# Optimization experiments

Hardware: AMD Instinct MI355X
Metric: run time of the kernel (lower is better)

The kernel has to match this reference:

```python
import jax, jax.numpy as jnp
import numpy as np

# norse LIFParameters defaults
ALPHA = 100.0        # superspike surrogate slope
DT = 1e-3
TAU_SYN_INV = 200.0  # 1/5e-3
TAU_MEM_INV = 100.0  # 1/1e-2
V_TH = 1.0           # v_leak = v_reset = 0

@jax.custom_vjp
def heaviside(v):
    # forward: hard threshold; backward: superspike surrogate 1/(alpha*|v|+1)^2
    return (v > 0).astype(v.dtype)

def _hv_fwd(v):
    return heaviside(v), v

def _hv_bwd(v, g):
    return (g / (ALPHA * jnp.abs(v) + 1.0) ** 2,)

heaviside.defvjp(_hv_fwd, _hv_bwd)

def setup_inputs() -> dict:
    key = jax.random.key(0)
    ks = jax.random.split(key, 5)
    B, H, W, O = 2048, 15, 15, 10
    x = jax.random.uniform(ks[0], (B, 1, H, W), jnp.float32)  # image-like in [0,1)
    conv_w = jax.random.normal(ks[1], (2, 1, 4, 4), jnp.float32) * 0.25
    conv_b = jax.random.normal(ks[2], (2,), jnp.float32) * 0.1
    lin_w = jax.random.normal(ks[3], (O, 72), jnp.float32) * (1.0 / np.sqrt(72.0))
    lin_b = jax.random.normal(ks[4], (O,), jnp.float32) * 0.1
    return {"x": x, "conv_w": conv_w, "conv_b": conv_b,
            "lin_w": lin_w, "lin_b": lin_b, "num_steps": 300}

def reference(x, conv_w, conv_b, lin_w, lin_b, num_steps):
    B = x.shape[0]
    O = lin_w.shape[0]
    current = x * 10.0  # constant input current to the encoder

    def step(carry, _):
        v_enc, v, i = carry
        # --- constant_current_lif_encode step (lif_current_encoder) ---
        v_enc = v_enc + DT * TAU_MEM_INV * (-v_enc + current)
        z_in = heaviside(v_enc - V_TH)
        v_enc = v_enc - z_in * v_enc  # reset to v_reset = 0
        # --- feed-forward: conv -> maxpool(2) -> linear ---
        c = jax.lax.conv_general_dilated(
            z_in, conv_w, (1, 1), 'VALID',
            dimension_numbers=('NCHW', 'OIHW', 'NCHW')) + conv_b[None, :, None, None]
        p = jax.lax.reduce_window(c, -jnp.inf, jax.lax.max,
                                  (1, 1, 2, 2), (1, 1, 2, 2), 'VALID')  # [B,2,6,6]
        lin = p.reshape(B, -1) @ lin_w.T + lin_b  # [B,O]
        # --- norse LIFCell (lif_feed_forward_step) ---
        v_dec = v + DT * TAU_MEM_INV * (-v + i)
        i_dec = i - DT * TAU_SYN_INV * i
        spk = heaviside(v_dec - V_TH)
        v_new = (1.0 - spk) * v_dec  # v_reset = 0
        i_new = i_dec + lin
        return (v_enc, v_new, i_new), (spk, v_new)

    init = (jnp.zeros_like(current),
            jnp.zeros((B, O), x.dtype),
            jnp.zeros((B, O), x.dtype))
    _, (spk_rec, mem_rec) = jax.lax.scan(step, init, None, length=num_steps)
    spk_out = spk_rec.sum(0)  # [B,O]
    return spk_out, mem_rec, spk_rec
```

## Files before the change

### kernel.cpp

```cpp
#include <hip/hip_runtime.h>
#include <math.h>


typedef float v2f __attribute__((ext_vector_type(2)));

__global__ __launch_bounds__(128, 4) void snn_step_kernel(
    const float* __restrict__ x,
    const float* __restrict__ conv_w,
    const float* __restrict__ conv_b,
    const float* __restrict__ lin_w,
    const float* __restrict__ lin_b,
    float* __restrict__ out,
    int T, int B)
{
    const int b   = blockIdx.x;
    const int tid = threadIdx.x;
    const int w   = tid & 63;
    const int wv  = tid >> 6;

    __shared__ float    s_linw[720];
    __shared__ float    s_linb[10];
    __shared__ float4   s_lut[4][32];
    __shared__ uint4    s_bits4[16][8];
    __shared__ float    s_p[16][80];

    for (int j = tid; j < 720; j += 128) s_linw[j] = lin_w[j];
    if (tid < 10) s_linb[tid] = lin_b[tid];
    {
        const int ky = tid >> 5, n = tid & 31;
        float s00 = 0.f, s01 = 0.f, s10 = 0.f, s11 = 0.f;
#pragma unroll
        for (int kx = 0; kx < 4; ++kx) {
            const float w0 = conv_w[ky * 4 + kx];
            const float w1 = conv_w[16 + ky * 4 + kx];
            if ((n >> kx) & 1)       { s00 += w0; s01 += w1; }
            if ((n >> (kx + 1)) & 1) { s10 += w0; s11 += w1; }
        }
        s_lut[ky][n] = make_float4(s00, s01, s10, s11);
    }
    __syncthreads();

    v2f ve01 = (v2f){0.f, 0.f}, ve23 = (v2f){0.f, 0.f};
    v2f cur01, cur23;
    {
        const int jrow = w >> 4, col = w & 15;
        float c[4];
#pragma unroll
        for (int k = 0; k < 4; ++k) {
            const int  row = 4 * k + jrow;
            const bool act = (col < 15) && (row < 15) && (wv == 0);
            c[k] = act ? __fmul_rn(x[(size_t)b * 225 + row * 15 + col], 10.0f) : 0.f;
        }
        cur01 = (v2f){c[0], c[1]};
        cur23 = (v2f){c[2], c[3]};
    }

    const int  jword   = (w >> 2) + (w & 3);
    const bool wr_bits = (w < 24);

    const bool convlane = (w < 36);
    const int  py = w / 6, px = w - 6 * py;
    const int  wordsel = py;
    const int  shx = 2 * px, shx16 = shx + 16;
    const int  poff = 20 * (w / 9) + 2 * (w - 9 * (w / 9));
    const v2f  cb2 = (v2f){conv_b[0], conv_b[1]};

    const int lo = w >> 2, lq = w & 3;
    v2f lw2[9];
#pragma unroll
    for (int t = 0; t < 9; ++t) {
        int i0 = lo * 72 + 9 * lq + t;
        int i1 = i0 + 36;
        lw2[t] = (v2f){s_linw[i0 < 720 ? i0 : 719],
                       s_linw[i1 < 720 ? i1 : 719]};
    }
    const float lbias = s_linb[lo < 10 ? lo : 0];
    float v = 0.f, i_syn = 0.f, sc = 0.f;
    float svv[6], svs[6];
    const size_t BO = (size_t)B * 10;
    float* mp  = out + BO + (size_t)b * 10 + lo;
    float* spp = out + BO + (size_t)T * BO + (size_t)b * 10 + lo;

    auto enc_pack = [&](int slot) {
        const v2f tenth = (v2f){0.1f, 0.1f};
        v2f vn01 = ve01 + (cur01 - ve01) * tenth;
        v2f vn23 = ve23 + (cur23 - ve23) * tenth;
        bool sp0 = (vn01.x > 1.0f);
        bool sp1 = (vn01.y > 1.0f);
        bool sp2 = (vn23.x > 1.0f);
        bool sp3 = (vn23.y > 1.0f);
        unsigned long long bal0 = __ballot(sp0);
        unsigned long long bal1 = __ballot(sp1);
        unsigned long long bal2 = __ballot(sp2);
        unsigned long long bal3 = __ballot(sp3);
        ve01 = (v2f){sp0 ? 0.f : vn01.x, sp1 ? 0.f : vn01.y};
        ve23 = (v2f){sp2 ? 0.f : vn23.x, sp3 ? 0.f : vn23.y};
        const int jh = jword >> 1;
        unsigned long long m01 = (jh & 1) ? bal1 : bal0;
        unsigned long long m23 = (jh & 1) ? bal3 : bal2;
        unsigned long long m   = (jh & 2) ? m23 : m01;
        unsigned word = (unsigned)((jword & 1) ? (m >> 32) : m);
        word = (jword < 8) ? word : 0u;
        if (wr_bits) ((unsigned*)&s_bits4[slot][0])[w] = word;
    };

    auto conv_compute = [&](int slot, unsigned wb0, unsigned wb1, unsigned wb2) {
        const int i0 = (wb0 >> shx)   & 31;
        const int i1 = (wb0 >> shx16) & 31;
        const int i2 = (wb1 >> shx)   & 31;
        const int i3 = (wb1 >> shx16) & 31;
        const int i4 = (wb2 >> shx)   & 31;

        const float4 f0 = s_lut[0][i0];
        const float4 f1 = s_lut[1][i1];
        const float4 f2 = s_lut[2][i2];
        const float4 f3 = s_lut[3][i3];
        const float4 g0 = s_lut[0][i1];
        const float4 g1 = s_lut[1][i2];
        const float4 g2 = s_lut[2][i3];
        const float4 g3 = s_lut[3][i4];

        v2f a00 = (v2f){f0.x, f0.y};  a00 += (v2f){f1.x, f1.y};
        a00 += (v2f){f2.x, f2.y};     a00 += (v2f){f3.x, f3.y};
        v2f a01 = (v2f){f0.z, f0.w};  a01 += (v2f){f1.z, f1.w};
        a01 += (v2f){f2.z, f2.w};     a01 += (v2f){f3.z, f3.w};
        v2f a10 = (v2f){g0.x, g0.y};  a10 += (v2f){g1.x, g1.y};
        a10 += (v2f){g2.x, g2.y};     a10 += (v2f){g3.x, g3.y};
        v2f a11 = (v2f){g0.z, g0.w};  a11 += (v2f){g1.z, g1.w};
        a11 += (v2f){g2.z, g2.w};     a11 += (v2f){g3.z, g3.w};

        v2f mraw = __builtin_elementwise_max(
                       __builtin_elementwise_max(a00, a01),
                       __builtin_elementwise_max(a10, a11));
        v2f m2 = mraw + cb2;

        *(v2f*)&s_p[slot][poff] = m2;
    };

    auto lin_dec = [&](int s, int k) {
        const float* base = &s_p[s & 15][lq * 20];
        float4 q0 = *(const float4*)(base + 0);
        float4 q1 = *(const float4*)(base + 4);
        float4 q2 = *(const float4*)(base + 8);
        float4 q3 = *(const float4*)(base + 12);
        v2f    q4 = *(const v2f*)(base + 16);
        v2f pacc = (v2f){0.f, 0.f};
        pacc = __builtin_elementwise_fma(lw2[0], (v2f){q0.x, q0.y}, pacc);
        pacc = __builtin_elementwise_fma(lw2[1], (v2f){q0.z, q0.w}, pacc);
        pacc = __builtin_elementwise_fma(lw2[2], (v2f){q1.x, q1.y}, pacc);
        pacc = __builtin_elementwise_fma(lw2[3], (v2f){q1.z, q1.w}, pacc);
        pacc = __builtin_elementwise_fma(lw2[4], (v2f){q2.x, q2.y}, pacc);
        pacc = __builtin_elementwise_fma(lw2[5], (v2f){q2.z, q2.w}, pacc);
        pacc = __builtin_elementwise_fma(lw2[6], (v2f){q3.x, q3.y}, pacc);
        pacc = __builtin_elementwise_fma(lw2[7], (v2f){q3.z, q3.w}, pacc);
        pacc = __builtin_elementwise_fma(lw2[8], q4, pacc);
        float partial = __fadd_rn(pacc.x, pacc.y);

        float p1 = __shfl_xor(partial, 1);
        float p2 = __shfl_xor(partial, 2);
        float p3 = __shfl_xor(partial, 3);
        float lin = __fadd_rn(
            __fadd_rn(__fadd_rn(__fadd_rn(partial, p1), p2), p3), lbias);

        float vd  = __fadd_rn(v, __fmul_rn(0.1f, __fsub_rn(i_syn, v)));
        float id  = __fsub_rn(i_syn, __fmul_rn(0.2f, i_syn));
        float spk = (vd > 1.0f) ? 1.0f : 0.0f;
        v = (vd > 1.0f) ? 0.0f : vd;
        sc += spk;
        svv[k] = v;
        svs[k] = spk;
        i_syn = __fadd_rn(id, lin);
    };

    auto issue_stores = [&]() {
        if (lq == 0 && lo < 10) {
#pragma unroll
            for (int k = 0; k < 6; ++k) {
                mp[(size_t)k * BO]  = svv[k];
                spp[(size_t)k * BO] = svs[k];
            }
        }
        mp  += 6 * BO;
        spp += 6 * BO;
    };

    if (wv == 0) enc_pack(0);

    const int NG = T / 6;

    for (int g = 0; g < NG; ++g) {
        const int base = 6 * g;
        if (wv == 0) {
#pragma unroll
            for (int k = 0; k < 4; ++k) {
                const int s = base + k;
                uint4 bb = make_uint4(0, 0, 0, 0);
                if (convlane) bb = s_bits4[s & 15][wordsel];
                enc_pack((s + 1) & 15);
                if (convlane) conv_compute(s & 15, bb.x, bb.y, bb.z);
            }
            enc_pack((base + 5) & 15);
            enc_pack((base + 6) & 15);
        } else {
            if (g >= 2) issue_stores();
            if (g >= 1) {
                const int pb = base - 6;
                if (convlane) {
                    uint4 ba = s_bits4[(pb + 4) & 15][wordsel];
                    uint4 bc = s_bits4[(pb + 5) & 15][wordsel];
                    conv_compute((pb + 4) & 15, ba.x, ba.y, ba.z);
                    conv_compute((pb + 5) & 15, bc.x, bc.y, bc.z);
                }
#pragma unroll
                for (int k = 0; k < 6; ++k)
                    lin_dec(pb + k, k);
            }
        }
        __syncthreads();
    }

    if (wv == 1) {
        issue_stores();
        const int pb = 6 * (NG - 1);
        if (convlane) {
            uint4 ba = s_bits4[(pb + 4) & 15][wordsel];
            uint4 bc = s_bits4[(pb + 5) & 15][wordsel];
            conv_compute((pb + 4) & 15, ba.x, ba.y, ba.z);
            conv_compute((pb + 5) & 15, bc.x, bc.y, bc.z);
        }
#pragma unroll
        for (int k = 0; k < 6; ++k)
            lin_dec(pb + k, k);
        issue_stores();
        if (lq == 0 && lo < 10) out[(size_t)b * 10 + lo] = sc;
    }
}

extern "C" void kernel_launch(void* const* d_in, const int* in_sizes, int n_in,
                              void* d_out, int out_size, void* d_ws, size_t ws_size,
                              hipStream_t stream) {
    const float* x      = (const float*)d_in[0];
    const float* conv_w = (const float*)d_in[1];
    const float* conv_b = (const float*)d_in[2];
    const float* lin_w  = (const float*)d_in[3];
    const float* lin_b  = (const float*)d_in[4];
    float* out = (float*)d_out;

    const int B = in_sizes[0] / 225;
    const int T = (out_size / (B * 10) - 1) / 2;

    snn_step_kernel<<<B, 128, 0, stream>>>(x, conv_w, conv_b, lin_w, lin_b, out, T, B);
}
```

Before: 201.9 us.

## Restructure two-wave pipeline: encode a full group ahead, software-pipeline linear loads, DPP reductions

Wave 0 now encodes six future timesteps per group (after a six-step prologue and barrier) and batches its bit loads ahead of the conv work. Wave 1 computes the conv for steps 4-5 of the current group instead of the previous one, which shortens the dependency lag. Its linear-layer LDS loads are split from the math so the next step's loads are issued before the current step's FMAs. The quad-lane shuffles become DPP quad-permute moves, which avoids LDS-backed shuffles. The cost is more live registers and a different inter-wave schedule whose correctness relies on the 16-slot ring indexing.

```diff
diff --git a/kernel.cpp b/kernel.cpp
--- a/kernel.cpp
+++ b/kernel.cpp
@@ -3,6 +3,9 @@
 
 
 typedef float v2f __attribute__((ext_vector_type(2)));
+
+#define DPPQ(x, ctrl) \
+    __int_as_float(__builtin_amdgcn_mov_dpp(__float_as_int(x), (ctrl), 0xf, 0xf, true))
 
 __global__ __launch_bounds__(128, 4) void snn_step_kernel(
     const float* __restrict__ x,
@@ -137,28 +140,35 @@
         *(v2f*)&s_p[slot][poff] = m2;
     };
 
-    auto lin_dec = [&](int s, int k) {
-        const float* base = &s_p[s & 15][lq * 20];
-        float4 q0 = *(const float4*)(base + 0);
-        float4 q1 = *(const float4*)(base + 4);
-        float4 q2 = *(const float4*)(base + 8);
-        float4 q3 = *(const float4*)(base + 12);
-        v2f    q4 = *(const v2f*)(base + 16);
+    struct LinLd { float4 q0, q1, q2, q3; v2f q4; };
+
+    auto lin_load = [&](int s) {
+        LinLd L;
+        const float* pbase = &s_p[s & 15][lq * 20];
+        L.q0 = *(const float4*)(pbase + 0);
+        L.q1 = *(const float4*)(pbase + 4);
+        L.q2 = *(const float4*)(pbase + 8);
+        L.q3 = *(const float4*)(pbase + 12);
+        L.q4 = *(const v2f*)(pbase + 16);
+        return L;
+    };
+
+    auto lin_math = [&](const LinLd& L, int k) {
         v2f pacc = (v2f){0.f, 0.f};
-        pacc = __builtin_elementwise_fma(lw2[0], (v2f){q0.x, q0.y}, pacc);
-        pacc = __builtin_elementwise_fma(lw2[1], (v2f){q0.z, q0.w}, pacc);
-        pacc = __builtin_elementwise_fma(lw2[2], (v2f){q1.x, q1.y}, pacc);
-        pacc = __builtin_elementwise_fma(lw2[3], (v2f){q1.z, q1.w}, pacc);
-        pacc = __builtin_elementwise_fma(lw2[4], (v2f){q2.x, q2.y}, pacc);
-        pacc = __builtin_elementwise_fma(lw2[5], (v2f){q2.z, q2.w}, pacc);
-        pacc = __builtin_elementwise_fma(lw2[6], (v2f){q3.x, q3.y}, pacc);
-        pacc = __builtin_elementwise_fma(lw2[7], (v2f){q3.z, q3.w}, pacc);
-        pacc = __builtin_elementwise_fma(lw2[8], q4, pacc);
+        pacc = __builtin_elementwise_fma(lw2[0], (v2f){L.q0.x, L.q0.y}, pacc);
+        pacc = __builtin_elementwise_fma(lw2[1], (v2f){L.q0.z, L.q0.w}, pacc);
+        pacc = __builtin_elementwise_fma(lw2[2], (v2f){L.q1.x, L.q1.y}, pacc);
+        pacc = __builtin_elementwise_fma(lw2[3], (v2f){L.q1.z, L.q1.w}, pacc);
+        pacc = __builtin_elementwise_fma(lw2[4], (v2f){L.q2.x, L.q2.y}, pacc);
+        pacc = __builtin_elementwise_fma(lw2[5], (v2f){L.q2.z, L.q2.w}, pacc);
+        pacc = __builtin_elementwise_fma(lw2[6], (v2f){L.q3.x, L.q3.y}, pacc);
+        pacc = __builtin_elementwise_fma(lw2[7], (v2f){L.q3.z, L.q3.w}, pacc);
+        pacc = __builtin_elementwise_fma(lw2[8], L.q4, pacc);
         float partial = __fadd_rn(pacc.x, pacc.y);
 
-        float p1 = __shfl_xor(partial, 1);
-        float p2 = __shfl_xor(partial, 2);
-        float p3 = __shfl_xor(partial, 3);
+        float p1 = DPPQ(partial, 177);
+        float p2 = DPPQ(partial, 78);
+        float p3 = DPPQ(partial, 27);
         float lin = __fadd_rn(
             __fadd_rn(__fadd_rn(__fadd_rn(partial, p1), p2), p3), lbias);
 
@@ -184,36 +194,61 @@
         spp += 6 * BO;
     };
 
-    if (wv == 0) enc_pack(0);
+    if (wv == 0) {
+        enc_pack(0); enc_pack(1); enc_pack(2);
+        enc_pack(3); enc_pack(4); enc_pack(5);
+    }
+    __syncthreads();
 
     const int NG = T / 6;
 
     for (int g = 0; g < NG; ++g) {
         const int base = 6 * g;
         if (wv == 0) {
-#pragma unroll
-            for (int k = 0; k < 4; ++k) {
-                const int s = base + k;
-                uint4 bb = make_uint4(0, 0, 0, 0);
-                if (convlane) bb = s_bits4[s & 15][wordsel];
-                enc_pack((s + 1) & 15);
-                if (convlane) conv_compute(s & 15, bb.x, bb.y, bb.z);
-            }
-            enc_pack((base + 5) & 15);
-            enc_pack((base + 6) & 15);
+            uint4 bb0 = make_uint4(0,0,0,0), bb1 = bb0, bb2 = bb0, bb3 = bb0;
+            if (convlane) {
+                bb0 = s_bits4[(base + 0) & 15][wordsel];
+                bb1 = s_bits4[(base + 1) & 15][wordsel];
+                bb2 = s_bits4[(base + 2) & 15][wordsel];
+                bb3 = s_bits4[(base + 3) & 15][wordsel];
+            }
+            enc_pack((base + 6)  & 15);
+            enc_pack((base + 7)  & 15);
+            enc_pack((base + 8)  & 15);
+            enc_pack((base + 9)  & 15);
+            enc_pack((base + 10) & 15);
+            enc_pack((base + 11) & 15);
+            if (convlane) {
+                conv_compute((base + 0) & 15, bb0.x, bb0.y, bb0.z);
+                conv_compute((base + 1) & 15, bb1.x, bb1.y, bb1.z);
+                conv_compute((base + 2) & 15, bb2.x, bb2.y, bb2.z);
+                conv_compute((base + 3) & 15, bb3.x, bb3.y, bb3.z);
+            }
         } else {
+            uint4 ba = make_uint4(0,0,0,0), bc = ba;
+            if (convlane) {
+                ba = s_bits4[(base + 4) & 15][wordsel];
+                bc = s_bits4[(base + 5) & 15][wordsel];
+            }
             if (g >= 2) issue_stores();
+            if (convlane) {
+                conv_compute((base + 4) & 15, ba.x, ba.y, ba.z);
+                conv_compute((base + 5) & 15, bc.x, bc.y, bc.z);
+            }
             if (g >= 1) {
                 const int pb = base - 6;
-                if (convlane) {
-                    uint4 ba = s_bits4[(pb + 4) & 15][wordsel];
-                    uint4 bc = s_bits4[(pb + 5) & 15][wordsel];
-                    conv_compute((pb + 4) & 15, ba.x, ba.y, ba.z);
-                    conv_compute((pb + 5) & 15, bc.x, bc.y, bc.z);
-                }
-#pragma unroll
-                for (int k = 0; k < 6; ++k)
-                    lin_dec(pb + k, k);
+                LinLd A0 = lin_load(pb + 0);
+                LinLd A1 = lin_load(pb + 1);
+                lin_math(A0, 0);
+                LinLd A2 = lin_load(pb + 2);
+                lin_math(A1, 1);
+                LinLd A3 = lin_load(pb + 3);
+                lin_math(A2, 2);
+                LinLd A4 = lin_load(pb + 4);
+                lin_math(A3, 3);
+                LinLd A5 = lin_load(pb + 5);
+                lin_math(A4, 4);
+                lin_math(A5, 5);
             }
         }
         __syncthreads();
@@ -221,16 +256,19 @@
 
     if (wv == 1) {
         issue_stores();
-        const int pb = 6 * (NG - 1);
-        if (convlane) {
-            uint4 ba = s_bits4[(pb + 4) & 15][wordsel];
-            uint4 bc = s_bits4[(pb + 5) & 15][wordsel];
-            conv_compute((pb + 4) & 15, ba.x, ba.y, ba.z);
-            conv_compute((pb + 5) & 15, bc.x, bc.y, bc.z);
-        }
-#pragma unroll
-        for (int k = 0; k < 6; ++k)
-            lin_dec(pb + k, k);
+        const int pb = T - 6;
+        LinLd A0 = lin_load(pb + 0);
+        LinLd A1 = lin_load(pb + 1);
+        lin_math(A0, 0);
+        LinLd A2 = lin_load(pb + 2);
+        lin_math(A1, 1);
+        LinLd A3 = lin_load(pb + 3);
+        lin_math(A2, 2);
+        LinLd A4 = lin_load(pb + 4);
+        lin_math(A3, 3);
+        LinLd A5 = lin_load(pb + 5);
+        lin_math(A4, 4);
+        lin_math(A5, 5);
         issue_stores();
         if (lq == 0 && lo < 10) out[(size_t)b * 10 + lo] = sc;
     }
```

After: 190.6 us. 5.6% less time.

## Exploit periodic encoder spikes to parallelize conv/linear across time chunks

Applied to the files above, without the earlier changes.

Each encoder pixel is driven by a constant current and resets to zero after a spike, so its spike train is exactly periodic. The kernel first finds each pixel's period, then generates spike bits directly from per-lane countdown counters. This lets four waves each run conv, maxpool and linear over a quarter of the time steps independently, writing the linear outputs into a shared buffer. A single wave then runs the sequential LIF recurrence and the output stores, and the quad reduction now uses DPP moves instead of shuffles. The cost is a 256-thread block, a larger shared buffer sized for 300 steps, and assumptions that T is a multiple of 4 and at most 300.

```diff
diff --git a/kernel.cpp b/kernel.cpp
--- a/kernel.cpp
+++ b/kernel.cpp
@@ -3,8 +3,12 @@
 
 
 typedef float v2f __attribute__((ext_vector_type(2)));
-
-__global__ __launch_bounds__(128, 4) void snn_step_kernel(
+typedef unsigned long long u64;
+
+#define DPPQ(x, ctrl) \
+    __int_as_float(__builtin_amdgcn_mov_dpp(__float_as_int(x), (ctrl), 0xf, 0xf, true))
+
+__global__ __launch_bounds__(256, 4) void snn_step_kernel(
     const float* __restrict__ x,
     const float* __restrict__ conv_w,
     const float* __restrict__ conv_b,
@@ -18,15 +22,12 @@
     const int w   = tid & 63;
     const int wv  = tid >> 6;
 
-    __shared__ float    s_linw[720];
-    __shared__ float    s_linb[10];
-    __shared__ float4   s_lut[4][32];
-    __shared__ uint4    s_bits4[16][8];
-    __shared__ float    s_p[16][80];
-
-    for (int j = tid; j < 720; j += 128) s_linw[j] = lin_w[j];
-    if (tid < 10) s_linb[tid] = lin_b[tid];
-    {
+    __shared__ float4         s_lut[4][32];
+    __shared__ unsigned short s_K[4][64];
+    __shared__ float          s_p[4][2][80];
+    __shared__ float          s_lin[300][10];
+
+    if (tid < 128) {
         const int ky = tid >> 5, n = tid & 31;
         float s00 = 0.f, s01 = 0.f, s10 = 0.f, s11 = 0.f;
 #pragma unroll
@@ -38,32 +39,37 @@
         }
         s_lut[ky][n] = make_float4(s00, s01, s10, s11);
     }
+
+    {
+        const int  row = 4 * wv + (w >> 4), col = w & 15;
+        const bool act = (col < 15) && (row < 15);
+        const float cur = act ? __fmul_rn(x[(size_t)b * 225 + row * 15 + col], 10.0f)
+                              : 0.f;
+        int   Kp = (cur > 1.0f) ? 0 : -1;
+        float ve = 0.f;
+        int t = 0;
+        while (t < T) {
+            if (__ballot(Kp == 0) == 0ull) break;
+#pragma unroll
+            for (int u = 0; u < 4; ++u) {
+                float vn = __fadd_rn(ve, __fmul_rn(0.1f, __fsub_rn(cur, ve)));
+                bool sp = (vn > 1.0f);
+                Kp = (Kp == 0 && sp) ? (t + u + 1) : Kp;
+                ve = sp ? 0.f : vn;
+            }
+            t += 4;
+        }
+        s_K[wv][w] = (unsigned short)(Kp > 0 ? Kp : 0);
+    }
     __syncthreads();
-
-    v2f ve01 = (v2f){0.f, 0.f}, ve23 = (v2f){0.f, 0.f};
-    v2f cur01, cur23;
-    {
-        const int jrow = w >> 4, col = w & 15;
-        float c[4];
-#pragma unroll
-        for (int k = 0; k < 4; ++k) {
-            const int  row = 4 * k + jrow;
-            const bool act = (col < 15) && (row < 15) && (wv == 0);
-            c[k] = act ? __fmul_rn(x[(size_t)b * 225 + row * 15 + col], 10.0f) : 0.f;
-        }
-        cur01 = (v2f){c[0], c[1]};
-        cur23 = (v2f){c[2], c[3]};
-    }
-
-    const int  jword   = (w >> 2) + (w & 3);
-    const bool wr_bits = (w < 24);
 
     const bool convlane = (w < 36);
     const int  py = w / 6, px = w - 6 * py;
-    const int  wordsel = py;
     const int  shx = 2 * px, shx16 = shx + 16;
     const int  poff = 20 * (w / 9) + 2 * (w - 9 * (w / 9));
     const v2f  cb2 = (v2f){conv_b[0], conv_b[1]};
+    const bool qe0 = ((py >> 1) == 0), qe1 = ((py >> 1) == 1);
+    const bool pyodd = (py & 1) != 0;
 
     const int lo = w >> 2, lq = w & 3;
     v2f lw2[9];
@@ -71,40 +77,32 @@
     for (int t = 0; t < 9; ++t) {
         int i0 = lo * 72 + 9 * lq + t;
         int i1 = i0 + 36;
-        lw2[t] = (v2f){s_linw[i0 < 720 ? i0 : 719],
-                       s_linw[i1 < 720 ? i1 : 719]};
-    }
-    const float lbias = s_linb[lo < 10 ? lo : 0];
-    float v = 0.f, i_syn = 0.f, sc = 0.f;
-    float svv[6], svs[6];
-    const size_t BO = (size_t)B * 10;
-    float* mp  = out + BO + (size_t)b * 10 + lo;
-    float* spp = out + BO + (size_t)T * BO + (size_t)b * 10 + lo;
-
-    auto enc_pack = [&](int slot) {
-        const v2f tenth = (v2f){0.1f, 0.1f};
-        v2f vn01 = ve01 + (cur01 - ve01) * tenth;
-        v2f vn23 = ve23 + (cur23 - ve23) * tenth;
-        bool sp0 = (vn01.x > 1.0f);
-        bool sp1 = (vn01.y > 1.0f);
-        bool sp2 = (vn23.x > 1.0f);
-        bool sp3 = (vn23.y > 1.0f);
-        unsigned long long bal0 = __ballot(sp0);
-        unsigned long long bal1 = __ballot(sp1);
-        unsigned long long bal2 = __ballot(sp2);
-        unsigned long long bal3 = __ballot(sp3);
-        ve01 = (v2f){sp0 ? 0.f : vn01.x, sp1 ? 0.f : vn01.y};
-        ve23 = (v2f){sp2 ? 0.f : vn23.x, sp3 ? 0.f : vn23.y};
-        const int jh = jword >> 1;
-        unsigned long long m01 = (jh & 1) ? bal1 : bal0;
-        unsigned long long m23 = (jh & 1) ? bal3 : bal2;
-        unsigned long long m   = (jh & 2) ? m23 : m01;
-        unsigned word = (unsigned)((jword & 1) ? (m >> 32) : m);
-        word = (jword < 8) ? word : 0u;
-        if (wr_bits) ((unsigned*)&s_bits4[slot][0])[w] = word;
+        lw2[t] = (v2f){lin_w[i0 < 720 ? i0 : 719], lin_w[i1 < 720 ? i1 : 719]};
+    }
+    const float lbias = lin_b[lo < 10 ? lo : 0];
+
+    const int Lc = T >> 2;
+    const int t0 = wv * Lc;
+
+    const int Ka = s_K[0][w], Kb = s_K[1][w], Kc = s_K[2][w], Kd = s_K[3][w];
+    int ca = Ka ? (Ka - 1 - t0 % Ka) : 0x0FFFFFFF;
+    int cb = Kb ? (Kb - 1 - t0 % Kb) : 0x0FFFFFFF;
+    int cc = Kc ? (Kc - 1 - t0 % Kc) : 0x0FFFFFFF;
+    int cd = Kd ? (Kd - 1 - t0 % Kd) : 0x0FFFFFFF;
+
+    auto enc_words = [&](unsigned& wb0, unsigned& wb1, unsigned& wb2) {
+        bool sp0 = (ca == 0); u64 b0 = __ballot(sp0); ca = sp0 ? (Ka - 1) : (ca - 1);
+        bool sp1 = (cb == 0); u64 b1 = __ballot(sp1); cb = sp1 ? (Kb - 1) : (cb - 1);
+        bool sp2 = (cc == 0); u64 b2 = __ballot(sp2); cc = sp2 ? (Kc - 1) : (cc - 1);
+        bool sp3 = (cd == 0); u64 b3 = __ballot(sp3); cd = sp3 ? (Kd - 1) : (cd - 1);
+        u64 balA = qe0 ? b0 : (qe1 ? b1 : b2);
+        u64 balB = qe0 ? b1 : (qe1 ? b2 : b3);
+        wb0 = pyodd ? (unsigned)(balA >> 32) : (unsigned)balA;
+        wb1 = pyodd ? (unsigned)balB         : (unsigned)(balA >> 32);
+        wb2 = pyodd ? (unsigned)(balB >> 32) : (unsigned)balB;
     };
 
-    auto conv_compute = [&](int slot, unsigned wb0, unsigned wb1, unsigned wb2) {
+    auto conv_compute = [&](int dbuf, unsigned wb0, unsigned wb1, unsigned wb2) {
         const int i0 = (wb0 >> shx)   & 31;
         const int i1 = (wb0 >> shx16) & 31;
         const int i2 = (wb1 >> shx)   & 31;
@@ -134,11 +132,11 @@
                        __builtin_elementwise_max(a10, a11));
         v2f m2 = mraw + cb2;
 
-        *(v2f*)&s_p[slot][poff] = m2;
+        *(v2f*)&s_p[wv][dbuf][poff] = m2;
     };
 
-    auto lin_dec = [&](int s, int k) {
-        const float* base = &s_p[s & 15][lq * 20];
+    auto lin_step = [&](int sm1) {
+        const float* base = &s_p[wv][sm1 & 1][lq * 20];
         float4 q0 = *(const float4*)(base + 0);
         float4 q1 = *(const float4*)(base + 4);
         float4 q2 = *(const float4*)(base + 8);
@@ -156,83 +154,49 @@
         pacc = __builtin_elementwise_fma(lw2[8], q4, pacc);
         float partial = __fadd_rn(pacc.x, pacc.y);
 
-        float p1 = __shfl_xor(partial, 1);
-        float p2 = __shfl_xor(partial, 2);
-        float p3 = __shfl_xor(partial, 3);
+        float p1 = DPPQ(partial, 177);
+        float p2 = DPPQ(partial, 78);
+        float p3 = DPPQ(partial, 27);
         float lin = __fadd_rn(
             __fadd_rn(__fadd_rn(__fadd_rn(partial, p1), p2), p3), lbias);
 
-        float vd  = __fadd_rn(v, __fmul_rn(0.1f, __fsub_rn(i_syn, v)));
-        float id  = __fsub_rn(i_syn, __fmul_rn(0.2f, i_syn));
-        float spk = (vd > 1.0f) ? 1.0f : 0.0f;
-        v = (vd > 1.0f) ? 0.0f : vd;
-        sc += spk;
-        svv[k] = v;
-        svs[k] = spk;
-        i_syn = __fadd_rn(id, lin);
+        if (lq == 0 && lo < 10) s_lin[t0 + sm1][lo] = lin;
     };
 
-    auto issue_stores = [&]() {
-        if (lq == 0 && lo < 10) {
-#pragma unroll
-            for (int k = 0; k < 6; ++k) {
-                mp[(size_t)k * BO]  = svv[k];
-                spp[(size_t)k * BO] = svs[k];
-            }
+    {
+        unsigned wb0, wb1, wb2;
+        enc_words(wb0, wb1, wb2);
+        if (convlane) conv_compute(0, wb0, wb1, wb2);
+    }
+    for (int s = 1; s < Lc; ++s) {
+        unsigned wb0, wb1, wb2;
+        enc_words(wb0, wb1, wb2);
+        if (convlane) conv_compute(s & 1, wb0, wb1, wb2);
+        lin_step(s - 1);
+    }
+    lin_step(Lc - 1);
+    __syncthreads();
+
+    if (wv == 0) {
+        float v = 0.f, i_syn = 0.f, sc = 0.f;
+        const int o = (w < 10) ? w : 0;
+        const size_t BO = (size_t)B * 10;
+        float* mp  = out + BO + (size_t)b * 10 + o;
+        float* spp = out + BO + (size_t)T * BO + (size_t)b * 10 + o;
+#pragma unroll 4
+        for (int t = 0; t < T; ++t) {
+            float lv  = s_lin[t][o];
+            float vd  = __fadd_rn(v, __fmul_rn(0.1f, __fsub_rn(i_syn, v)));
+            float id  = __fsub_rn(i_syn, __fmul_rn(0.2f, i_syn));
+            float spk = (vd > 1.0f) ? 1.0f : 0.0f;
+            v = (vd > 1.0f) ? 0.0f : vd;
+            sc += spk;
+            i_syn = __fadd_rn(id, lv);
+            if (w < 10) { *mp = v; *spp = spk; }
+            mp  += BO;
+            spp += BO;
         }
-        mp  += 6 * BO;
-        spp += 6 * BO;
-    };
-
-    if (wv == 0) enc_pack(0);
-
-    const int NG = T / 6;
-
-    for (int g = 0; g < NG; ++g) {
-        const int base = 6 * g;
-        if (wv == 0) {
-#pragma unroll
-            for (int k = 0; k < 4; ++k) {
-                const int s = base + k;
-                uint4 bb = make_uint4(0, 0, 0, 0);
-                if (convlane) bb = s_bits4[s & 15][wordsel];
-                enc_pack((s + 1) & 15);
-                if (convlane) conv_compute(s & 15, bb.x, bb.y, bb.z);
-            }
-            enc_pack((base + 5) & 15);
-            enc_pack((base + 6) & 15);
-        } else {
-            if (g >= 2) issue_stores();
-            if (g >= 1) {
-                const int pb = base - 6;
-                if (convlane) {
-                    uint4 ba = s_bits4[(pb + 4) & 15][wordsel];
-                    uint4 bc = s_bits4[(pb + 5) & 15][wordsel];
-                    conv_compute((pb + 4) & 15, ba.x, ba.y, ba.z);
-                    conv_compute((pb + 5) & 15, bc.x, bc.y, bc.z);
-                }
-#pragma unroll
-                for (int k = 0; k < 6; ++k)
-                    lin_dec(pb + k, k);
-            }
-        }
-        __syncthreads();
-    }
-
-    if (wv == 1) {
-        issue_stores();
-        const int pb = 6 * (NG - 1);
-        if (convlane) {
-            uint4 ba = s_bits4[(pb + 4) & 15][wordsel];
-            uint4 bc = s_bits4[(pb + 5) & 15][wordsel];
-            conv_compute((pb + 4) & 15, ba.x, ba.y, ba.z);
-            conv_compute((pb + 5) & 15, bc.x, bc.y, bc.z);
-        }
-#pragma unroll
-        for (int k = 0; k < 6; ++k)
-            lin_dec(pb + k, k);
-        issue_stores();
-        if (lq == 0 && lo < 10) out[(size_t)b * 10 + lo] = sc;
+        if (w < 10) out[(size_t)b * 10 + w] = sc;
     }
 }
 
@@ -249,5 +213,5 @@
     const int B = in_sizes[0] / 225;
     const int T = (out_size / (B * 10) - 1) / 2;
 
-    snn_step_kernel<<<B, 128, 0, stream>>>(x, conv_w, conv_b, lin_w, lin_b, out, T, B);
+    snn_step_kernel<<<B, 256, 0, stream>>>(x, conv_w, conv_b, lin_w, lin_b, out, T, B);
 }
```

New measurement: 188.9 us. -6.5%, faster.
